# Kernel tuning notes

Hardware: AMD Instinct MI355X
Metric: run time of the kernel (lower is better)

The kernel has to match this reference:

```python
import jax, jax.numpy as jnp
import numpy as np

E, H, F, N, B = 512, 8, 2048, 1024, 4
HD = E // H


def setup_inputs() -> dict:
    key = jax.random.key(0)
    ks = jax.random.split(key, 20)
    s = 0.02
    return {
        "node_inputs": jax.random.normal(ks[0], (N, B, E), jnp.float32),
        "parent_mask": jax.random.uniform(ks[1], (B, N, N), jnp.float32),
        "hidden": jax.random.bernoulli(ks[2], 0.5, (B, N, N)),
        "pad_mask": jax.random.bernoulli(ks[3], 0.1, (B, N)),
        "Wp": jax.random.normal(ks[4], (H, E), jnp.float32) * s,
        "bp": jnp.zeros((H,), jnp.float32),
        "Wc": jax.random.normal(ks[5], (H, E), jnp.float32) * s,
        "bc": jnp.zeros((H,), jnp.float32),
        "Wqkv": jax.random.normal(ks[6], (3 * E, E), jnp.float32) * s,
        "bqkv": jnp.zeros((3 * E,), jnp.float32),
        "Wo": jax.random.normal(ks[7], (E, E), jnp.float32) * s,
        "bo": jnp.zeros((E,), jnp.float32),
        "W1": jax.random.normal(ks[8], (F, E), jnp.float32) * s,
        "b1": jnp.zeros((F,), jnp.float32),
        "W2": jax.random.normal(ks[9], (E, F), jnp.float32) * s,
        "b2": jnp.zeros((E,), jnp.float32),
        "ln1_g": jnp.ones((E,), jnp.float32),
        "ln1_b": jnp.zeros((E,), jnp.float32),
        "ln2_g": jnp.ones((E,), jnp.float32),
        "ln2_b": jnp.zeros((E,), jnp.float32),
    }


def _layer_norm(x, g, b, eps=1e-5):
    m = jnp.mean(x, axis=-1, keepdims=True)
    v = jnp.mean((x - m) ** 2, axis=-1, keepdims=True)
    return (x - m) * jax.lax.rsqrt(v + eps) * g + b


def reference(node_inputs, parent_mask, hidden, pad_mask, Wp, bp, Wc, bc,
              Wqkv, bqkv, Wo, bo, W1, b1, W2, b2, ln1_g, ln1_b, ln2_g, ln2_b):
    x = node_inputs  # (N, B, E), seq-first like nn.TransformerEncoderLayer
    # parent/child per-head biases: Linear(E->H), permuted to (B, H, N)
    pbias = jnp.transpose(x @ Wp.T + bp, (1, 2, 0))
    cbias = jnp.transpose(x @ Wc.T + bc, (1, 2, 0))
    # additive attention bias (B, H, N, N)
    am = (jnp.swapaxes(parent_mask, 1, 2)[:, None] * pbias[..., None]
          + parent_mask[:, None] * cbias[..., None])
    am = jnp.where(hidden[:, None], -jnp.inf, am)
    # multi-head self-attention
    qkv = x @ Wqkv.T + bqkv  # (N, B, 3E)
    q, k, v = jnp.split(qkv, 3, axis=-1)

    def heads(t):  # (N, B, E) -> (B, H, N, HD)
        return jnp.transpose(t.reshape(N, B, H, HD), (1, 2, 0, 3))

    q, k, v = heads(q), heads(k), heads(v)
    scores = jnp.einsum("bhqd,bhkd->bhqk", q, k) / jnp.sqrt(jnp.float32(HD)) + am
    scores = jnp.where(pad_mask[:, None, None, :], -jnp.inf, scores)
    attn = jax.nn.softmax(scores, axis=-1)
    ctx = jnp.einsum("bhqk,bhkd->bhqd", attn, v)  # (B, H, N, HD)
    ctx = jnp.transpose(ctx, (2, 0, 1, 3)).reshape(N, B, E)
    attn_out = ctx @ Wo.T + bo
    # post-norm transformer encoder layer (dropout=0, relu activation)
    y = _layer_norm(x + attn_out, ln1_g, ln1_b)
    ff = jax.nn.relu(y @ W1.T + b1) @ W2.T + b2
    return _layer_norm(y + ff, ln2_g, ln2_b)
```

## Files before the change

### kernel.cpp

```cpp
#include <hip/hip_runtime.h>
#include <hip/hip_bf16.h>
#include <stdint.h>

using bf16 = __hip_bfloat16;

typedef __bf16 bf16x8 __attribute__((ext_vector_type(8)));
typedef float  f32x4  __attribute__((ext_vector_type(4)));

__device__ __forceinline__ float bflo(uint32_t u) { return __uint_as_float(u << 16); }
__device__ __forceinline__ float bfhi(uint32_t u) { return __uint_as_float(u & 0xffff0000u); }

__device__ __forceinline__ void load8(const bf16* p, float* f) {
  uint4 u = *(const uint4*)p;
  f[0] = bflo(u.x); f[1] = bfhi(u.x);
  f[2] = bflo(u.y); f[3] = bfhi(u.y);
  f[4] = bflo(u.z); f[5] = bfhi(u.z);
  f[6] = bflo(u.w); f[7] = bfhi(u.w);
}
__device__ __forceinline__ void load8(const float* p, float* f) {
  float4 a = *(const float4*)p, b = *(const float4*)(p + 4);
  f[0] = a.x; f[1] = a.y; f[2] = a.z; f[3] = a.w;
  f[4] = b.x; f[5] = b.y; f[6] = b.z; f[7] = b.w;
}
__device__ __forceinline__ void store1(float* o, float v) { *o = v; }
__device__ __forceinline__ void store1(bf16* o, float v) { *o = __float2bfloat16(v); }
__device__ __forceinline__ uint32_t bfbits(float x) {
  bf16 v = __float2bfloat16(x);
  return (uint32_t)*(uint16_t*)&v;
}

typedef const uint32_t __attribute__((address_space(1)))* gp_t;
typedef uint32_t __attribute__((address_space(3)))* lp_t;
__device__ __forceinline__ void gload16(const void* g, void* l) {
  __builtin_amdgcn_global_load_lds((gp_t)g, (lp_t)l, 16, 0, 0);
}

__global__ __launch_bounds__(256)
void cvt5(const float* __restrict__ s0, const float* __restrict__ s1,
          const float* __restrict__ s2, const float* __restrict__ s3,
          const float* __restrict__ s4, bf16* __restrict__ d0,
          bf16* __restrict__ d1, bf16* __restrict__ d2,
          bf16* __restrict__ d3, bf16* __restrict__ d4)
{
  size_t j = ((size_t)blockIdx.x * 256 + threadIdx.x) * 8;
  const float* s; bf16* o; size_t off;
  if      (j < 2097152) { s = s0; o = d0; off = j; }
  else if (j < 2883584) { s = s1; o = d1; off = j - 2097152; }
  else if (j < 3145728) { s = s2; o = d2; off = j - 2883584; }
  else if (j < 4194304) { s = s3; o = d3; off = j - 3145728; }
  else                  { s = s4; o = d4; off = j - 4194304; }
  float f[8];
  load8(s + off, f);
  uint4 u;
  u.x = (bfbits(f[1]) << 16) | bfbits(f[0]);
  u.y = (bfbits(f[3]) << 16) | bfbits(f[2]);
  u.z = (bfbits(f[5]) << 16) | bfbits(f[4]);
  u.w = (bfbits(f[7]) << 16) | bfbits(f[6]);
  *(uint4*)(o + off) = u;
}

__global__ __launch_bounds__(256)
void mask_pack(const float* __restrict__ pm, const int* __restrict__ hid,
               const int* __restrict__ padm, uint32_t* __restrict__ out)
{
  __shared__ float tileT[128][65];
  const int b = blockIdx.z, q0 = blockIdx.y * 64, k0 = blockIdx.x * 128;
  const int t = threadIdx.x;
  const size_t pb = (size_t)b << 20;
#pragma unroll
  for (int i = 0; i < 32; ++i) {
    int idx = t + i * 256;
    int r = idx >> 6, c = idx & 63;
    tileT[r][c] = pm[pb + (size_t)(k0 + r) * 1024 + q0 + c];
  }
  __syncthreads();
#pragma unroll
  for (int i = 0; i < 32; ++i) {
    int idx = t + i * 256;
    int q = idx >> 7, pos = idx & 127;
    int k = (pos & 7) * 16 + (pos >> 3);
    size_t src = pb + (size_t)(q0 + q) * 1024 + k0 + k;
    int msk = hid[src] | padm[b * 1024 + k0 + k];
    uint32_t u = 0xFFFFFFFFu;
    if (!msk) u = (bfbits(tileT[k][q]) << 16) | bfbits(pm[src]);
    out[pb + (size_t)(q0 + q) * 1024 + k0 + pos] = u;
  }
}

template<int MODE, int BN>
__global__ __launch_bounds__(256)
void gemm_bt(const bf16* __restrict__ A, const bf16* __restrict__ W,
             const float* __restrict__ bias, bf16* __restrict__ outb,
             int M, int Nout, int K)
{
  constexpr int NT = BN / 32;
  __shared__ bf16 As[128 * 64];
  __shared__ bf16 Bs[BN * 64];
  const int t = threadIdx.x, lane = t & 63, wave = t >> 6;
  const int m0 = blockIdx.y * 128, n0 = blockIdx.x * BN;
  const int wr = wave >> 1, wc = wave & 1;
  const int frow = lane & 15, ksel = (lane >> 4) * 8;
  f32x4 acc[4 * NT] = {};
  const bf16* Ab = A + (size_t)m0 * K;
  const bf16* Wb = W + (size_t)n0 * K;

  for (int k0 = 0; k0 < K; k0 += 64) {
    __syncthreads();
#pragma unroll
    for (int i = 0; i < 4; ++i) {
      int ib = i * 256 + wave * 64;
      int idx = ib + lane;
      gload16(Ab + (size_t)(idx >> 3) * K + k0 + (idx & 7) * 8, As + ib * 8);
    }
#pragma unroll
    for (int i = 0; i < BN / 32; ++i) {
      int ib = i * 256 + wave * 64;
      int idx = ib + lane;
      gload16(Wb + (size_t)(idx >> 3) * K + k0 + (idx & 7) * 8, Bs + ib * 8);
    }
    __syncthreads();
#pragma unroll
    for (int kk = 0; kk < 64; kk += 32) {
      bf16x8 af[4], bf_[NT];
#pragma unroll
      for (int mt = 0; mt < 4; ++mt)
        af[mt] = *(const bf16x8*)(As + (wr * 64 + mt * 16 + frow) * 64 + kk + ksel);
#pragma unroll
      for (int nt = 0; nt < NT; ++nt)
        bf_[nt] = *(const bf16x8*)(Bs + (wc * (BN / 2) + nt * 16 + frow) * 64 + kk + ksel);
#pragma unroll
      for (int mt = 0; mt < 4; ++mt)
#pragma unroll
        for (int nt = 0; nt < NT; ++nt)
          acc[mt * NT + nt] = __builtin_amdgcn_mfma_f32_16x16x32_bf16(
              af[mt], bf_[nt], acc[mt * NT + nt], 0, 0, 0);
    }
  }
  const int rb = (lane >> 4) * 4, cb = lane & 15;
#pragma unroll
  for (int mt = 0; mt < 4; ++mt)
#pragma unroll
    for (int nt = 0; nt < NT; ++nt) {
      f32x4 a = acc[mt * NT + nt];
#pragma unroll
      for (int r = 0; r < 4; ++r) {
        int row = m0 + wr * 64 + mt * 16 + rb + r;
        int col = n0 + wc * (BN / 2) + nt * 16 + cb;
        float v = a[r] + bias[col];
        if (MODE == 1) v = fmaxf(v, 0.f);
        if (MODE == 2) {
          int which = col >> 9, hh = (col >> 6) & 7, d = col & 63;
          int n = row >> 2, b = row & 3;
          size_t idx;
          if (which == 2)
            idx = (((size_t)(64 + b * 8 + hh)) << 16) + (size_t)d * 1024 + n;
          else
            idx = (((size_t)(which * 32 + b * 8 + hh)) << 16) + (size_t)n * 64 + d;
          outb[idx] = __float2bfloat16(v);
        } else {
          outb[(size_t)row * Nout + col] = __float2bfloat16(v);
        }
      }
    }
}

__global__ __launch_bounds__(256)
void pbcb_kernel(const float* __restrict__ x, const float* __restrict__ Wp,
                 const float* __restrict__ bp, const float* __restrict__ Wc,
                 const float* __restrict__ bc, float* __restrict__ pbo,
                 float* __restrict__ cbo)
{
  const int wave = threadIdx.x >> 6, lane = threadIdx.x & 63;
  const int m = blockIdx.x * 4 + wave;
  float xv[8];
  load8(x + (size_t)m * 512 + lane * 8, xv);
  const int n = m >> 2, b = m & 3;
#pragma unroll
  for (int hh = 0; hh < 8; ++hh) {
    float wp[8], wc[8];
    load8(Wp + (size_t)hh * 512 + lane * 8, wp);
    load8(Wc + (size_t)hh * 512 + lane * 8, wc);
    float ap = 0.f, ac = 0.f;
#pragma unroll
    for (int j = 0; j < 8; ++j) { ap += xv[j] * wp[j]; ac += xv[j] * wc[j]; }
#pragma unroll
    for (int off = 32; off; off >>= 1) {
      ap += __shfl_xor(ap, off);
      ac += __shfl_xor(ac, off);
    }
    if (lane == 0) {
      pbo[((size_t)b * 8 + hh) * 1024 + n] = ap + bp[hh];
      cbo[((size_t)b * 8 + hh) * 1024 + n] = ac + bc[hh];
    }
  }
}

__global__ __launch_bounds__(256, 3)
void attn_mfma(const bf16* __restrict__ qkv, const float* __restrict__ pbw,
               const float* __restrict__ cbw, const uint32_t* __restrict__ mpk,
               bf16* __restrict__ ctxo)
{
  __shared__ bf16 Kt[128][72];
  __shared__ bf16 Vt[64][136];
  __shared__ bf16 Ps[4][16][136];
  const int t = threadIdx.x, lane = t & 63, wave = t >> 6;
  const int g = lane >> 4, c = lane & 15;
  const int h = blockIdx.y, b = blockIdx.z;
  const int q0 = blockIdx.x * 64 + wave * 16;
  const size_t bh = (size_t)b * 8 + h;
  const bf16* Qp = qkv + (bh << 16);
  const bf16* Kp = qkv + ((32 + bh) << 16);
  const bf16* Vg = qkv + ((64 + bh) << 16);

  bf16x8 qa0 = *(const bf16x8*)(Qp + (size_t)(q0 + c) * 64 + g * 8);
  bf16x8 qa1 = *(const bf16x8*)(Qp + (size_t)(q0 + c) * 64 + 32 + g * 8);

  float pbq[4], cbq[4];
#pragma unroll
  for (int r = 0; r < 4; ++r) {
    pbq[r] = pbw[bh * 1024 + q0 + 4 * g + r];
    cbq[r] = cbw[bh * 1024 + q0 + 4 * g + r];
  }
  const uint32_t* mbase = mpk + (((size_t)b * 1024 + q0 + 4 * g) << 10) + c * 8;

  f32x4 oacc[4] = {{0,0,0,0},{0,0,0,0},{0,0,0,0},{0,0,0,0}};
  float mrow[4] = {-1e30f,-1e30f,-1e30f,-1e30f};
  float lrow[4] = {0.f,0.f,0.f,0.f};

  for (int kt = 0; kt < 8; ++kt) {
    const int k0 = kt * 128;
    __syncthreads();
#pragma unroll
    for (int i = 0; i < 4; ++i) {
      int idx = t + i * 256;
      int r = idx >> 3, cc = idx & 7;
      *(uint4*)&Kt[r][cc * 8] = *(const uint4*)(Kp + (size_t)(k0 + r) * 64 + cc * 8);
    }
#pragma unroll
    for (int i = 0; i < 4; ++i) {
      int idx = t + i * 256;
      int r = idx >> 4, cc = idx & 15;
      *(uint4*)&Vt[r][cc * 8] = *(const uint4*)(Vg + (size_t)r * 1024 + k0 + cc * 8);
    }
    __syncthreads();
    f32x4 sacc[8];
#pragma unroll
    for (int nt = 0; nt < 8; ++nt) {
      f32x4 z = {0.f,0.f,0.f,0.f};
      bf16x8 k0f = *(const bf16x8*)&Kt[nt * 16 + c][g * 8];
      bf16x8 k1f = *(const bf16x8*)&Kt[nt * 16 + c][32 + g * 8];
      z = __builtin_amdgcn_mfma_f32_16x16x32_bf16(qa0, k0f, z, 0, 0, 0);
      z = __builtin_amdgcn_mfma_f32_16x16x32_bf16(qa1, k1f, z, 0, 0, 0);
      sacc[nt] = z;
    }
    float al[4];
#pragma unroll
    for (int r = 0; r < 4; ++r) {
      const uint32_t* mp = mbase + ((size_t)r << 10) + k0;
      uint4 u0 = *(const uint4*)mp;
      uint4 u1 = *(const uint4*)(mp + 4);
      uint32_t uu[8] = {u0.x, u0.y, u0.z, u0.w, u1.x, u1.y, u1.z, u1.w};
      float sv[8];
      float mx = -1e30f;
#pragma unroll
      for (int nt = 0; nt < 8; ++nt) {
        float s = sacc[nt][r] * 0.125f + bfhi(uu[nt]) * pbq[r] + bflo(uu[nt]) * cbq[r];
        s = (uu[nt] == 0xFFFFFFFFu) ? -1e30f : s;
        sv[nt] = s;
        mx = fmaxf(mx, s);
      }
#pragma unroll
      for (int off = 8; off; off >>= 1) mx = fmaxf(mx, __shfl_xor(mx, off));
      float newm = fmaxf(mrow[r], mx);
      al[r] = __expf(mrow[r] - newm);
      float ps = 0.f;
#pragma unroll
      for (int nt = 0; nt < 8; ++nt) {
        float p = (sv[nt] <= -1e29f) ? 0.f : __expf(sv[nt] - newm);
        ps += p;
        Ps[wave][4 * g + r][nt * 16 + c] = __float2bfloat16(p);
      }
#pragma unroll
      for (int off = 8; off; off >>= 1) ps += __shfl_xor(ps, off);
      lrow[r] = lrow[r] * al[r] + ps;
      mrow[r] = newm;
    }
    {
      int srcl = (c >> 2) * 16;
      float a0 = __shfl(al[0], srcl), a1 = __shfl(al[1], srcl);
      float a2 = __shfl(al[2], srcl), a3 = __shfl(al[3], srcl);
      int rr = c & 3;
      float aq = rr == 0 ? a0 : rr == 1 ? a1 : rr == 2 ? a2 : a3;
#pragma unroll
      for (int dt = 0; dt < 4; ++dt) {
        oacc[dt][0] *= aq; oacc[dt][1] *= aq;
        oacc[dt][2] *= aq; oacc[dt][3] *= aq;
      }
    }
#pragma unroll
    for (int dt = 0; dt < 4; ++dt) {
#pragma unroll
      for (int kc = 0; kc < 4; ++kc) {
        bf16x8 vf = *(const bf16x8*)&Vt[dt * 16 + c][kc * 32 + g * 8];
        bf16x8 pf = *(const bf16x8*)&Ps[wave][c][kc * 32 + g * 8];
        oacc[dt] = __builtin_amdgcn_mfma_f32_16x16x32_bf16(vf, pf, oacc[dt], 0, 0, 0);
      }
    }
  }
  float lq;
  {
    int srcl = (c >> 2) * 16;
    float l0 = __shfl(lrow[0], srcl), l1 = __shfl(lrow[1], srcl);
    float l2 = __shfl(lrow[2], srcl), l3 = __shfl(lrow[3], srcl);
    int rr = c & 3;
    lq = rr == 0 ? l0 : rr == 1 ? l1 : rr == 2 ? l2 : l3;
  }
  const float inv = (lq > 0.f) ? 1.f / lq : 0.f;
  const int qg = q0 + c;
#pragma unroll
  for (int dt = 0; dt < 4; ++dt)
#pragma unroll
    for (int rg = 0; rg < 4; ++rg) {
      int d = dt * 16 + 4 * g + rg;
      ctxo[((size_t)qg * 4 + b) * 512 + h * 64 + d] =
          __float2bfloat16(oacc[dt][rg] * inv);
    }
}

template<typename TA, typename TR, typename TO>
__global__ __launch_bounds__(256)
void ln_res(const TA* __restrict__ a, const TR* __restrict__ rsd,
            const float* __restrict__ g, const float* __restrict__ be,
            TO* __restrict__ out)
{
  const int wave = threadIdx.x >> 6, lane = threadIdx.x & 63;
  const int m = blockIdx.x * 4 + wave;
  const size_t base = (size_t)m * 512 + lane * 8;
  float va[8], vb[8];
  load8(a + base, va);
  load8(rsd + base, vb);
  float v[8], s = 0.f;
#pragma unroll
  for (int j = 0; j < 8; ++j) { v[j] = va[j] + vb[j]; s += v[j]; }
#pragma unroll
  for (int off = 32; off; off >>= 1) s += __shfl_xor(s, off);
  const float mean = s * (1.f / 512.f);
  float q = 0.f;
#pragma unroll
  for (int j = 0; j < 8; ++j) { float d = v[j] - mean; q += d * d; }
#pragma unroll
  for (int off = 32; off; off >>= 1) q += __shfl_xor(q, off);
  const float rs = rsqrtf(q * (1.f / 512.f) + 1e-5f);
  float gv[8], bv[8];
  load8(g + lane * 8, gv);
  load8(be + lane * 8, bv);
#pragma unroll
  for (int j = 0; j < 8; ++j)
    store1(out + base + j, (v[j] - mean) * rs * gv[j] + bv[j]);
}

extern "C" void kernel_launch(void* const* d_in, const int* in_sizes, int n_in,
                              void* d_out, int out_size, void* d_ws, size_t ws_size,
                              hipStream_t stream)
{
  (void)in_sizes; (void)n_in; (void)out_size; (void)ws_size;
  const float* x    = (const float*)d_in[0];
  const float* pm   = (const float*)d_in[1];
  const int*   hid  = (const int*)d_in[2];
  const int*   padm = (const int*)d_in[3];
  const float* Wp   = (const float*)d_in[4];
  const float* bp   = (const float*)d_in[5];
  const float* Wc   = (const float*)d_in[6];
  const float* bc   = (const float*)d_in[7];
  const float* Wqkv = (const float*)d_in[8];
  const float* bqkv = (const float*)d_in[9];
  const float* Wo   = (const float*)d_in[10];
  const float* bo   = (const float*)d_in[11];
  const float* W1   = (const float*)d_in[12];
  const float* b1   = (const float*)d_in[13];
  const float* W2   = (const float*)d_in[14];
  const float* b2   = (const float*)d_in[15];
  const float* g1   = (const float*)d_in[16];
  const float* be1  = (const float*)d_in[17];
  const float* g2   = (const float*)d_in[18];
  const float* be2  = (const float*)d_in[19];

  char* ws = (char*)d_ws;
  bf16*     qkvb  = (bf16*)    (ws);
  float*    pbo   = (float*)   (ws + 12582912);
  float*    cbo   = (float*)   (ws + 12713984);
  uint32_t* mpk   = (uint32_t*)(ws + 12845056);
  bf16*     ctx   = (bf16*)    (ws + 29622272);
  bf16*     attno = (bf16*)    (ws + 33816576);
  bf16*     y     = (bf16*)    (ws + 38010880);
  bf16*     xb    = (bf16*)    (ws + 42205184);
  bf16*     wqkvb = (bf16*)    (ws + 46399488);
  bf16*     wob   = (bf16*)    (ws + 47972352);
  bf16*     w1b   = (bf16*)    (ws + 48496640);
  bf16*     w2b   = (bf16*)    (ws + 50593792);
  bf16*     ff1   = (bf16*)    (ws);
  bf16*     ff2   = (bf16*)    (ws + 29622272);

  cvt5<<<2560, 256, 0, stream>>>(x, Wqkv, Wo, W1, W2, xb, wqkvb, wob, w1b, w2b);
  mask_pack<<<dim3(8, 16, 4), 256, 0, stream>>>(pm, hid, padm, mpk);
  pbcb_kernel<<<1024, 256, 0, stream>>>(x, Wp, bp, Wc, bc, pbo, cbo);
  gemm_bt<2, 128><<<dim3(12, 32), 256, 0, stream>>>(xb, wqkvb, bqkv, qkvb, 4096, 1536, 512);
  attn_mfma<<<dim3(16, 8, 4), 256, 0, stream>>>(qkvb, pbo, cbo, mpk, ctx);
  gemm_bt<0, 64><<<dim3(8, 32), 256, 0, stream>>>(ctx, wob, bo, attno, 4096, 512, 512);
  ln_res<float, bf16, bf16><<<1024, 256, 0, stream>>>(x, attno, g1, be1, y);
  gemm_bt<1, 128><<<dim3(16, 32), 256, 0, stream>>>(y, w1b, b1, ff1, 4096, 2048, 512);
  gemm_bt<0, 64><<<dim3(8, 32), 256, 0, stream>>>(ff1, w2b, b2, ff2, 4096, 512, 2048);
  ln_res<bf16, bf16, float><<<1024, 256, 0, stream>>>(y, ff2, g2, be2, (float*)d_out);
}
```

Before: 301.5 us.

## Split-K the output GEMMs, transpose attention scores for per-lane rows, simplify mask layout

The Wo and W2 GEMMs become split-K with two partial fp32 outputs. A new LayerNorm kernel sums both partials with the bias and residual, which doubles the block count of these small GEMMs. The attention kernel swaps the MFMA operands so each lane owns one query row. That removes the cross-lane row shuffles, and the mask now loads as contiguous uint4 vectors. The mask_pack output layout becomes plain row-major, and LDS padding and occupancy bounds change. The cost is extra fp32 partial traffic and lower attention occupancy.

```diff
diff --git a/kernel.cpp b/kernel.cpp
--- a/kernel.cpp
+++ b/kernel.cpp
@@ -77,13 +77,12 @@
 #pragma unroll
   for (int i = 0; i < 32; ++i) {
     int idx = t + i * 256;
-    int q = idx >> 7, pos = idx & 127;
-    int k = (pos & 7) * 16 + (pos >> 3);
+    int q = idx >> 7, k = idx & 127;
     size_t src = pb + (size_t)(q0 + q) * 1024 + k0 + k;
     int msk = hid[src] | padm[b * 1024 + k0 + k];
     uint32_t u = 0xFFFFFFFFu;
     if (!msk) u = (bfbits(tileT[k][q]) << 16) | bfbits(pm[src]);
-    out[pb + (size_t)(q0 + q) * 1024 + k0 + pos] = u;
+    out[src] = u;
   }
 }
 
@@ -91,20 +90,22 @@
 __global__ __launch_bounds__(256)
 void gemm_bt(const bf16* __restrict__ A, const bf16* __restrict__ W,
              const float* __restrict__ bias, bf16* __restrict__ outb,
-             int M, int Nout, int K)
+             float* __restrict__ outf, int M, int Nout, int K, int kLen)
 {
   constexpr int NT = BN / 32;
   __shared__ bf16 As[128 * 64];
   __shared__ bf16 Bs[BN * 64];
   const int t = threadIdx.x, lane = t & 63, wave = t >> 6;
   const int m0 = blockIdx.y * 128, n0 = blockIdx.x * BN;
+  const int kOff = blockIdx.z * kLen;
+  if (MODE == 3) outf += (size_t)blockIdx.z * M * Nout;
   const int wr = wave >> 1, wc = wave & 1;
   const int frow = lane & 15, ksel = (lane >> 4) * 8;
   f32x4 acc[4 * NT] = {};
   const bf16* Ab = A + (size_t)m0 * K;
   const bf16* Wb = W + (size_t)n0 * K;
 
-  for (int k0 = 0; k0 < K; k0 += 64) {
+  for (int k0 = kOff; k0 < kOff + kLen; k0 += 64) {
     __syncthreads();
 #pragma unroll
     for (int i = 0; i < 4; ++i) {
@@ -146,19 +147,23 @@
       for (int r = 0; r < 4; ++r) {
         int row = m0 + wr * 64 + mt * 16 + rb + r;
         int col = n0 + wc * (BN / 2) + nt * 16 + cb;
-        float v = a[r] + bias[col];
-        if (MODE == 1) v = fmaxf(v, 0.f);
-        if (MODE == 2) {
-          int which = col >> 9, hh = (col >> 6) & 7, d = col & 63;
-          int n = row >> 2, b = row & 3;
-          size_t idx;
-          if (which == 2)
-            idx = (((size_t)(64 + b * 8 + hh)) << 16) + (size_t)d * 1024 + n;
-          else
-            idx = (((size_t)(which * 32 + b * 8 + hh)) << 16) + (size_t)n * 64 + d;
-          outb[idx] = __float2bfloat16(v);
+        if (MODE == 3) {
+          outf[(size_t)row * Nout + col] = a[r];
         } else {
-          outb[(size_t)row * Nout + col] = __float2bfloat16(v);
+          float v = a[r] + bias[col];
+          if (MODE == 1) v = fmaxf(v, 0.f);
+          if (MODE == 2) {
+            int which = col >> 9, hh = (col >> 6) & 7, d = col & 63;
+            int n = row >> 2, b = row & 3;
+            size_t idx;
+            if (which == 2)
+              idx = (((size_t)(64 + b * 8 + hh)) << 16) + (size_t)d * 1024 + n;
+            else
+              idx = (((size_t)(which * 32 + b * 8 + hh)) << 16) + (size_t)n * 64 + d;
+            outb[idx] = __float2bfloat16(v);
+          } else {
+            outb[(size_t)row * Nout + col] = __float2bfloat16(v);
+          }
         }
       }
     }
@@ -195,14 +200,14 @@
   }
 }
 
-__global__ __launch_bounds__(256, 3)
+__global__ __launch_bounds__(256, 2)
 void attn_mfma(const bf16* __restrict__ qkv, const float* __restrict__ pbw,
                const float* __restrict__ cbw, const uint32_t* __restrict__ mpk,
                bf16* __restrict__ ctxo)
 {
-  __shared__ bf16 Kt[128][72];
-  __shared__ bf16 Vt[64][136];
-  __shared__ bf16 Ps[4][16][136];
+  __shared__ bf16 Kt[128][80];
+  __shared__ bf16 Vt[64][144];
+  __shared__ bf16 Ps[4][16][144];
   const int t = threadIdx.x, lane = t & 63, wave = t >> 6;
   const int g = lane >> 4, c = lane & 15;
   const int h = blockIdx.y, b = blockIdx.z;
@@ -215,20 +220,19 @@
   bf16x8 qa0 = *(const bf16x8*)(Qp + (size_t)(q0 + c) * 64 + g * 8);
   bf16x8 qa1 = *(const bf16x8*)(Qp + (size_t)(q0 + c) * 64 + 32 + g * 8);
 
-  float pbq[4], cbq[4];
-#pragma unroll
-  for (int r = 0; r < 4; ++r) {
-    pbq[r] = pbw[bh * 1024 + q0 + 4 * g + r];
-    cbq[r] = cbw[bh * 1024 + q0 + 4 * g + r];
-  }
-  const uint32_t* mbase = mpk + (((size_t)b * 1024 + q0 + 4 * g) << 10) + c * 8;
+  const float pbq = pbw[bh * 1024 + q0 + c];
+  const float cbq = cbw[bh * 1024 + q0 + c];
+  const uint32_t* mrp = mpk + (((size_t)b * 1024 + q0 + c) << 10);
 
   f32x4 oacc[4] = {{0,0,0,0},{0,0,0,0},{0,0,0,0},{0,0,0,0}};
-  float mrow[4] = {-1e30f,-1e30f,-1e30f,-1e30f};
-  float lrow[4] = {0.f,0.f,0.f,0.f};
+  float m = -1e30f, l = 0.f;
 
   for (int kt = 0; kt < 8; ++kt) {
     const int k0 = kt * 128;
+    uint4 mu[8];
+#pragma unroll
+    for (int nt = 0; nt < 8; ++nt)
+      mu[nt] = *(const uint4*)(mrp + k0 + nt * 16 + 4 * g);
     __syncthreads();
 #pragma unroll
     for (int i = 0; i < 4; ++i) {
@@ -249,53 +253,47 @@
       f32x4 z = {0.f,0.f,0.f,0.f};
       bf16x8 k0f = *(const bf16x8*)&Kt[nt * 16 + c][g * 8];
       bf16x8 k1f = *(const bf16x8*)&Kt[nt * 16 + c][32 + g * 8];
-      z = __builtin_amdgcn_mfma_f32_16x16x32_bf16(qa0, k0f, z, 0, 0, 0);
-      z = __builtin_amdgcn_mfma_f32_16x16x32_bf16(qa1, k1f, z, 0, 0, 0);
+      z = __builtin_amdgcn_mfma_f32_16x16x32_bf16(k0f, qa0, z, 0, 0, 0);
+      z = __builtin_amdgcn_mfma_f32_16x16x32_bf16(k1f, qa1, z, 0, 0, 0);
       sacc[nt] = z;
     }
-    float al[4];
-#pragma unroll
-    for (int r = 0; r < 4; ++r) {
-      const uint32_t* mp = mbase + ((size_t)r << 10) + k0;
-      uint4 u0 = *(const uint4*)mp;
-      uint4 u1 = *(const uint4*)(mp + 4);
-      uint32_t uu[8] = {u0.x, u0.y, u0.z, u0.w, u1.x, u1.y, u1.z, u1.w};
-      float sv[8];
-      float mx = -1e30f;
-#pragma unroll
-      for (int nt = 0; nt < 8; ++nt) {
-        float s = sacc[nt][r] * 0.125f + bfhi(uu[nt]) * pbq[r] + bflo(uu[nt]) * cbq[r];
-        s = (uu[nt] == 0xFFFFFFFFu) ? -1e30f : s;
-        sv[nt] = s;
+    float mx = -1e30f;
+#pragma unroll
+    for (int nt = 0; nt < 8; ++nt) {
+      uint32_t uu[4] = {mu[nt].x, mu[nt].y, mu[nt].z, mu[nt].w};
+#pragma unroll
+      for (int r = 0; r < 4; ++r) {
+        float s = sacc[nt][r] * 0.125f + bfhi(uu[r]) * pbq + bflo(uu[r]) * cbq;
+        s = (uu[r] == 0xFFFFFFFFu) ? -1e30f : s;
+        sacc[nt][r] = s;
         mx = fmaxf(mx, s);
       }
-#pragma unroll
-      for (int off = 8; off; off >>= 1) mx = fmaxf(mx, __shfl_xor(mx, off));
-      float newm = fmaxf(mrow[r], mx);
-      al[r] = __expf(mrow[r] - newm);
-      float ps = 0.f;
-#pragma unroll
-      for (int nt = 0; nt < 8; ++nt) {
-        float p = (sv[nt] <= -1e29f) ? 0.f : __expf(sv[nt] - newm);
-        ps += p;
-        Ps[wave][4 * g + r][nt * 16 + c] = __float2bfloat16(p);
-      }
-#pragma unroll
-      for (int off = 8; off; off >>= 1) ps += __shfl_xor(ps, off);
-      lrow[r] = lrow[r] * al[r] + ps;
-      mrow[r] = newm;
-    }
-    {
-      int srcl = (c >> 2) * 16;
-      float a0 = __shfl(al[0], srcl), a1 = __shfl(al[1], srcl);
-      float a2 = __shfl(al[2], srcl), a3 = __shfl(al[3], srcl);
-      int rr = c & 3;
-      float aq = rr == 0 ? a0 : rr == 1 ? a1 : rr == 2 ? a2 : a3;
-#pragma unroll
-      for (int dt = 0; dt < 4; ++dt) {
-        oacc[dt][0] *= aq; oacc[dt][1] *= aq;
-        oacc[dt][2] *= aq; oacc[dt][3] *= aq;
-      }
+    }
+    mx = fmaxf(mx, __shfl_xor(mx, 16));
+    mx = fmaxf(mx, __shfl_xor(mx, 32));
+    const float newm = fmaxf(m, mx);
+    const float al = __expf(m - newm);
+    float ps = 0.f;
+#pragma unroll
+    for (int nt = 0; nt < 8; ++nt) {
+      float p0 = (sacc[nt][0] <= -1e29f) ? 0.f : __expf(sacc[nt][0] - newm);
+      float p1 = (sacc[nt][1] <= -1e29f) ? 0.f : __expf(sacc[nt][1] - newm);
+      float p2 = (sacc[nt][2] <= -1e29f) ? 0.f : __expf(sacc[nt][2] - newm);
+      float p3 = (sacc[nt][3] <= -1e29f) ? 0.f : __expf(sacc[nt][3] - newm);
+      ps += (p0 + p1) + (p2 + p3);
+      uint2 w;
+      w.x = (bfbits(p1) << 16) | bfbits(p0);
+      w.y = (bfbits(p3) << 16) | bfbits(p2);
+      *(uint2*)&Ps[wave][c][nt * 16 + 4 * g] = w;
+    }
+    ps += __shfl_xor(ps, 16);
+    ps += __shfl_xor(ps, 32);
+    l = l * al + ps;
+    m = newm;
+#pragma unroll
+    for (int dt = 0; dt < 4; ++dt) {
+      oacc[dt][0] *= al; oacc[dt][1] *= al;
+      oacc[dt][2] *= al; oacc[dt][3] *= al;
     }
 #pragma unroll
     for (int dt = 0; dt < 4; ++dt) {
@@ -307,15 +305,7 @@
       }
     }
   }
-  float lq;
-  {
-    int srcl = (c >> 2) * 16;
-    float l0 = __shfl(lrow[0], srcl), l1 = __shfl(lrow[1], srcl);
-    float l2 = __shfl(lrow[2], srcl), l3 = __shfl(lrow[3], srcl);
-    int rr = c & 3;
-    lq = rr == 0 ? l0 : rr == 1 ? l1 : rr == 2 ? l2 : l3;
-  }
-  const float inv = (lq > 0.f) ? 1.f / lq : 0.f;
+  const float inv = (l > 0.f) ? 1.f / l : 0.f;
   const int qg = q0 + c;
 #pragma unroll
   for (int dt = 0; dt < 4; ++dt)
@@ -327,21 +317,24 @@
     }
 }
 
-template<typename TA, typename TR, typename TO>
+template<typename TA, typename TO>
 __global__ __launch_bounds__(256)
-void ln_res(const TA* __restrict__ a, const TR* __restrict__ rsd,
-            const float* __restrict__ g, const float* __restrict__ be,
-            TO* __restrict__ out)
+void ln_res2(const TA* __restrict__ a, const float* __restrict__ p0,
+             const float* __restrict__ p1, const float* __restrict__ bias,
+             const float* __restrict__ g, const float* __restrict__ be,
+             TO* __restrict__ out)
 {
   const int wave = threadIdx.x >> 6, lane = threadIdx.x & 63;
   const int m = blockIdx.x * 4 + wave;
   const size_t base = (size_t)m * 512 + lane * 8;
-  float va[8], vb[8];
+  float va[8], f0[8], f1[8], bb[8];
   load8(a + base, va);
-  load8(rsd + base, vb);
+  load8(p0 + base, f0);
+  load8(p1 + base, f1);
+  load8(bias + lane * 8, bb);
   float v[8], s = 0.f;
 #pragma unroll
-  for (int j = 0; j < 8; ++j) { v[j] = va[j] + vb[j]; s += v[j]; }
+  for (int j = 0; j < 8; ++j) { v[j] = va[j] + f0[j] + f1[j] + bb[j]; s += v[j]; }
 #pragma unroll
   for (int off = 32; off; off >>= 1) s += __shfl_xor(s, off);
   const float mean = s * (1.f / 512.f);
@@ -391,24 +384,24 @@
   float*    cbo   = (float*)   (ws + 12713984);
   uint32_t* mpk   = (uint32_t*)(ws + 12845056);
   bf16*     ctx   = (bf16*)    (ws + 29622272);
-  bf16*     attno = (bf16*)    (ws + 33816576);
-  bf16*     y     = (bf16*)    (ws + 38010880);
-  bf16*     xb    = (bf16*)    (ws + 42205184);
-  bf16*     wqkvb = (bf16*)    (ws + 46399488);
-  bf16*     wob   = (bf16*)    (ws + 47972352);
-  bf16*     w1b   = (bf16*)    (ws + 48496640);
-  bf16*     w2b   = (bf16*)    (ws + 50593792);
-  bf16*     ff1   = (bf16*)    (ws);
-  bf16*     ff2   = (bf16*)    (ws + 29622272);
+  float*    part  = (float*)   (ws);
+  bf16*     ff1   = (bf16*)    (ws + 16777216);
+  bf16*     y     = (bf16*)    (ws + 33816576);
+  bf16*     xb    = (bf16*)    (ws + 38010880);
+  bf16*     wqkvb = (bf16*)    (ws + 42205184);
+  bf16*     wob   = (bf16*)    (ws + 43778048);
+  bf16*     w1b   = (bf16*)    (ws + 44302336);
+  bf16*     w2b   = (bf16*)    (ws + 46399488);
+  float*    part1 = part + (size_t)4096 * 512;
 
   cvt5<<<2560, 256, 0, stream>>>(x, Wqkv, Wo, W1, W2, xb, wqkvb, wob, w1b, w2b);
   mask_pack<<<dim3(8, 16, 4), 256, 0, stream>>>(pm, hid, padm, mpk);
   pbcb_kernel<<<1024, 256, 0, stream>>>(x, Wp, bp, Wc, bc, pbo, cbo);
-  gemm_bt<2, 128><<<dim3(12, 32), 256, 0, stream>>>(xb, wqkvb, bqkv, qkvb, 4096, 1536, 512);
+  gemm_bt<2, 128><<<dim3(12, 32), 256, 0, stream>>>(xb, wqkvb, bqkv, qkvb, nullptr, 4096, 1536, 512, 512);
   attn_mfma<<<dim3(16, 8, 4), 256, 0, stream>>>(qkvb, pbo, cbo, mpk, ctx);
-  gemm_bt<0, 64><<<dim3(8, 32), 256, 0, stream>>>(ctx, wob, bo, attno, 4096, 512, 512);
-  ln_res<float, bf16, bf16><<<1024, 256, 0, stream>>>(x, attno, g1, be1, y);
-  gemm_bt<1, 128><<<dim3(16, 32), 256, 0, stream>>>(y, w1b, b1, ff1, 4096, 2048, 512);
-  gemm_bt<0, 64><<<dim3(8, 32), 256, 0, stream>>>(ff1, w2b, b2, ff2, 4096, 512, 2048);
-  ln_res<bf16, bf16, float><<<1024, 256, 0, stream>>>(y, ff2, g2, be2, (float*)d_out);
-}
+  gemm_bt<3, 64><<<dim3(8, 32, 2), 256, 0, stream>>>(ctx, wob, nullptr, nullptr, part, 4096, 512, 512, 256);
+  ln_res2<float, bf16><<<1024, 256, 0, stream>>>(x, part, part1, bo, g1, be1, y);
+  gemm_bt<1, 128><<<dim3(16, 32), 256, 0, stream>>>(y, w1b, b1, ff1, nullptr, 4096, 2048, 512, 512);
+  gemm_bt<3, 64><<<dim3(8, 32, 2), 256, 0, stream>>>(ff1, w2b, nullptr, nullptr, part, 4096, 512, 2048, 1024);
+  ln_res2<bf16, float><<<1024, 256, 0, stream>>>(y, part, part1, b2, g2, be2, (float*)d_out);
+}
```

Result: faster. 278.8 us (-7.5%).
